# Performance work log

Hardware: AMD Instinct MI355X
Metric: run time of the kernel (lower is better)

Reference implementation:

```python
import jax, jax.numpy as jnp
import numpy as np

# dims
B, N, C_A, C_S, C_Z = 2, 8192, 128, 384, 16
H, D = 4, 32            # n_heads, head_dim (H*D == C_A)
NQ, NK = 32, 128        # local window: queries / keys
NB = 3                  # n_blocks
W = N // NQ             # number of query windows
HID = 2 * C_A           # transition expansion (n=2)


def _ln(x, eps=1e-5):
    # LayerNorm without affine params
    m = jnp.mean(x, axis=-1, keepdims=True)
    v = jnp.var(x, axis=-1, keepdims=True)
    return (x - m) * jax.lax.rsqrt(v + eps)


def setup_inputs() -> dict:
    key = jax.random.key(0)
    ks = iter(jax.random.split(key, 40))
    def rn(shape, scale=1.0):
        return jax.random.normal(next(ks), shape, dtype=jnp.float32) * jnp.float32(scale)
    inp = {
        'q': rn((B, N, C_A)),
        's': rn((B, N, C_S)),
        'p': rn((B, W, NQ, NK, C_Z)),
        # AttentionPairBias (AF3 Alg 24) params, stacked over blocks
        'adaln_scale_w': rn((NB, C_S, C_A), C_S ** -0.5),
        'adaln_scale_b': jnp.zeros((NB, C_A), jnp.float32),
        'adaln_shift_w': rn((NB, C_S, C_A), C_S ** -0.5),
        'wq': rn((NB, C_A, H * D), C_A ** -0.5),
        'bq': jnp.zeros((NB, H * D), jnp.float32),
        'wk': rn((NB, C_A, H * D), C_A ** -0.5),
        'wv': rn((NB, C_A, H * D), C_A ** -0.5),
        'lnz_w': jnp.ones((NB, C_Z), jnp.float32),
        'lnz_b': jnp.zeros((NB, C_Z), jnp.float32),
        'wb_pair': rn((NB, C_Z, H), C_Z ** -0.5),
        'wg': rn((NB, C_A, H * D), C_A ** -0.5),
        'wo': rn((NB, H * D, C_A), (H * D) ** -0.5),
        'sgate_w': rn((NB, C_S, C_A), C_S ** -0.5),
        'sgate_b': jnp.full((NB, C_A), -2.0, jnp.float32),
        # ConditionedTransitionBlock (AF3 Alg 25) params
        't_scale_w': rn((NB, C_S, C_A), C_S ** -0.5),
        't_scale_b': jnp.zeros((NB, C_A), jnp.float32),
        't_shift_w': rn((NB, C_S, C_A), C_S ** -0.5),
        't_wa': rn((NB, C_A, HID), C_A ** -0.5),
        't_wb': rn((NB, C_A, HID), C_A ** -0.5),
        't_wo': rn((NB, HID, C_A), HID ** -0.5),
        't_sgate_w': rn((NB, C_S, C_A), C_S ** -0.5),
        't_sgate_b': jnp.full((NB, C_A), -2.0, jnp.float32),
    }
    return inp


def reference(q, s, p,
              adaln_scale_w, adaln_scale_b, adaln_shift_w,
              wq, bq, wk, wv, lnz_w, lnz_b, wb_pair, wg, wo, sgate_w, sgate_b,
              t_scale_w, t_scale_b, t_shift_w, t_wa, t_wb, t_wo, t_sgate_w, t_sgate_b):
    a = q
    s_ln = _ln(s)  # [B, N, C_S], shared across blocks
    # local window key indices: window w covers queries [w*NQ, (w+1)*NQ), keys
    # are a centered NK-wide window -> offsets in [-(NK-NQ)//2, ...)
    off = (NK - NQ) // 2
    idx = jnp.arange(W)[:, None] * NQ - off + jnp.arange(NK)[None, :]  # [W, NK]
    valid = (idx >= 0) & (idx < N)
    idx_c = jnp.clip(idx, 0, N - 1)
    inv_sqrt_d = jnp.float32(1.0 / np.sqrt(D))
    NEG = jnp.float32(-1e9)

    for i in range(NB):
        # ---- AttentionPairBias (AdaLN-conditioned, pair-biased, gated) ----
        a_ln = _ln(a)
        a_ln = jax.nn.sigmoid(s_ln @ adaln_scale_w[i] + adaln_scale_b[i]) * a_ln \
               + s_ln @ adaln_shift_w[i]
        qh = (a_ln @ wq[i] + bq[i]).reshape(B, N, H, D)
        kh = (a_ln @ wk[i]).reshape(B, N, H, D)
        vh = (a_ln @ wv[i]).reshape(B, N, H, D)
        g = jax.nn.sigmoid(a_ln @ wg[i]).reshape(B, N, H, D)
        # pair bias from z: LN + linear to heads -> [B, W, NQ, NK, H]
        bias = (_ln(p) * lnz_w[i] + lnz_b[i]) @ wb_pair[i]
        qw = qh.reshape(B, W, NQ, H, D)
        kw = kh[:, idx_c]  # [B, W, NK, H, D]
        vw = vh[:, idx_c]
        logits = jnp.einsum('bwqhd,bwkhd->bwqkh', qw, kw) * inv_sqrt_d + bias
        logits = jnp.where(valid[None, :, None, :, None], logits, NEG)
        attn = jax.nn.softmax(logits, axis=3)
        ow = jnp.einsum('bwqkh,bwkhd->bwqhd', attn, vw)
        o = (g * ow.reshape(B, N, H, D)).reshape(B, N, H * D)
        attn_out = (o @ wo[i]) * jax.nn.sigmoid(s_ln @ sgate_w[i] + sgate_b[i])
        # ---- ConditionedTransitionBlock (SwiGLU, sigmoid-gated) ----
        t_ln = _ln(a)
        t_ln = jax.nn.sigmoid(s_ln @ t_scale_w[i] + t_scale_b[i]) * t_ln \
               + s_ln @ t_shift_w[i]
        hidden = jax.nn.silu(t_ln @ t_wa[i]) * (t_ln @ t_wb[i])
        trans_out = (hidden @ t_wo[i]) * jax.nn.sigmoid(s_ln @ t_sgate_w[i] + t_sgate_b[i])
        # AF3 Alg 23: a <- b + ConditionedTransitionBlock(a, s)
        a = attn_out + trans_out
    return a
```

## Files before the change

kernel.cpp:

```cpp
#include <hip/hip_runtime.h>
#include <hip/hip_bf16.h>
#include <cstddef>
#include <cstdint>

#define BB   2
#define NN   8192
#define CA   128
#define CS   384
#define CZ   16
#define HH   4
#define DD   32
#define NQW  32
#define NKW  128
#define NBLK 3
#define WW   256
#define MR   (BB*NN)
#define HIDN 256

typedef unsigned short u16;
typedef __attribute__((ext_vector_type(8))) short short8;
typedef __attribute__((ext_vector_type(4))) float floatx4;

__device__ __forceinline__ float sigmoidf_(float x) { return 1.f / (1.f + __expf(-x)); }

__device__ __forceinline__ u16 f2bf(float x) {
  unsigned u = __float_as_uint(x);
  unsigned r = (u + 0x7fffu + ((u >> 16) & 1u)) >> 16;
  return (u16)r;
}
__device__ __forceinline__ float bf2f(u16 u) {
  return __uint_as_float(((unsigned)u) << 16);
}

__global__ __launch_bounds__(256) void ln_s_kernel(const float* __restrict__ s,
                                                   u16* __restrict__ s_ln_bf) {
  int row  = blockIdx.x * 4 + (threadIdx.x >> 6);
  int lane = threadIdx.x & 63;
  const float* sr = s + (size_t)row * CS;
  float x[6];
  float sum = 0.f, sq = 0.f;
#pragma unroll
  for (int t = 0; t < 6; ++t) { x[t] = sr[lane + 64*t]; sum += x[t]; sq += x[t]*x[t]; }
#pragma unroll
  for (int off = 32; off; off >>= 1) { sum += __shfl_down(sum, off); sq += __shfl_down(sq, off); }
  sum = __shfl(sum, 0); sq = __shfl(sq, 0);
  float mean = sum * (1.f/CS);
  float var  = sq  * (1.f/CS) - mean*mean;
  float rstd = rsqrtf(var + 1e-5f);
  u16* orow = s_ln_bf + (size_t)row * CS;
#pragma unroll
  for (int t = 0; t < 6; ++t) orow[lane + 64*t] = f2bf((x[t]-mean)*rstd);
}

__global__ __launch_bounds__(256) void modln_kernel(const float* __restrict__ a,
                                                    const u16* __restrict__ sp0,
                                                    const u16* __restrict__ sp1,
                                                    const u16* __restrict__ sp3,
                                                    const u16* __restrict__ sp4,
                                                    u16* __restrict__ amod,
                                                    u16* __restrict__ tmod) {
  int row  = blockIdx.x * 4 + (threadIdx.x >> 6);
  int lane = threadIdx.x & 63;
  const float* ar = a + (size_t)row * CA;
  float x0 = ar[lane], x1 = ar[lane + 64];
  float sum = x0 + x1, sq = x0*x0 + x1*x1;
#pragma unroll
  for (int off = 32; off; off >>= 1) { sum += __shfl_down(sum, off); sq += __shfl_down(sq, off); }
  sum = __shfl(sum, 0); sq = __shfl(sq, 0);
  float mean = sum * (1.f/CA);
  float var  = sq  * (1.f/CA) - mean*mean;
  float rstd = rsqrtf(var + 1e-5f);
  float n0 = (x0-mean)*rstd, n1 = (x1-mean)*rstd;
  size_t i0 = (size_t)row * CA + lane;
  amod[i0]      = f2bf(bf2f(sp0[i0])     *n0 + bf2f(sp1[i0]));
  amod[i0 + 64] = f2bf(bf2f(sp0[i0 + 64])*n1 + bf2f(sp1[i0 + 64]));
  tmod[i0]      = f2bf(bf2f(sp3[i0])     *n0 + bf2f(sp4[i0]));
  tmod[i0 + 64] = f2bf(bf2f(sp3[i0 + 64])*n1 + bf2f(sp4[i0 + 64]));
}

struct TJob { const float* src; u16* dst; int K; int N; };
struct TJobs { TJob j[42]; };

__global__ __launch_bounds__(256) void transpose_bf16(TJobs jobs) {
  TJob jb = jobs.j[blockIdx.z];
  int tk = blockIdx.x * 32, tn = blockIdx.y * 32;
  if (tk >= jb.K || tn >= jb.N) return;
  __shared__ float tile[32][33];
  int tx = threadIdx.x & 31;
  int ty = threadIdx.x >> 5;
#pragma unroll
  for (int r = ty; r < 32; r += 8) tile[r][tx] = jb.src[(size_t)(tk + r) * jb.N + tn + tx];
  __syncthreads();
#pragma unroll
  for (int r = ty; r < 32; r += 8)
    jb.dst[(size_t)(tn + r) * jb.K + tk + tx] = f2bf(tile[tx][r]);
}

struct GemmJob {
  const u16* A;
  const u16* Bt;
  const u16* Bt2;
  const float* bias;
  u16* outbf;
  int K;
  int ostride;
  int mode;
  int pad;
};
struct GemmJobs { GemmJob j[18]; };

#define CH_STRIDE 1032

template <bool DUAL>
__global__ __launch_bounds__(256) void gemm_mfma(GemmJobs jobs) {
  GemmJob jb = jobs.j[blockIdx.z];
  const int bm = blockIdx.y * 128, bn = blockIdx.x * 128;
  const int K = jb.K;

  __shared__ u16 As[4 * CH_STRIDE];
  __shared__ u16 Bs[4 * CH_STRIDE];
  __shared__ u16 Bs2[DUAL ? 4 * CH_STRIDE : 8];

  const int tid  = threadIdx.x;
  const int lane = tid & 63;
  const int wave = tid >> 6;
  const int wr = wave >> 1, wc = wave & 1;
  const int l15 = lane & 15, quad = lane >> 4;

  floatx4 acc[4][4] = {};
  floatx4 acc2[DUAL ? 4 : 1][DUAL ? 4 : 1] = {};

  for (int k0 = 0; k0 < K; k0 += 32) {
    __syncthreads();
#pragma unroll
    for (int h = 0; h < 2; ++h) {
      int f = tid + 256 * h;
      int m = f >> 2, c = f & 3;
      uint4 av = *(const uint4*)(jb.A + (size_t)(bm + m) * K + k0 + c * 8);
      *(uint4*)(As + c * CH_STRIDE + m * 8) = av;
      uint4 bv = *(const uint4*)(jb.Bt + (size_t)(bn + m) * K + k0 + c * 8);
      *(uint4*)(Bs + c * CH_STRIDE + m * 8) = bv;
      if constexpr (DUAL) {
        uint4 bv2 = *(const uint4*)(jb.Bt2 + (size_t)(bn + m) * K + k0 + c * 8);
        *(uint4*)(Bs2 + c * CH_STRIDE + m * 8) = bv2;
      }
    }
    __syncthreads();

    short8 a_frag[4], b_frag[4];
#pragma unroll
    for (int mt = 0; mt < 4; ++mt)
      a_frag[mt] = *(const short8*)(As + quad * CH_STRIDE + (wr * 64 + mt * 16 + l15) * 8);
#pragma unroll
    for (int nt = 0; nt < 4; ++nt)
      b_frag[nt] = *(const short8*)(Bs + quad * CH_STRIDE + (wc * 64 + nt * 16 + l15) * 8);
#pragma unroll
    for (int mt = 0; mt < 4; ++mt)
#pragma unroll
      for (int nt = 0; nt < 4; ++nt)
        acc[mt][nt] = __builtin_amdgcn_mfma_f32_16x16x32_bf16(a_frag[mt], b_frag[nt], acc[mt][nt], 0, 0, 0);
    if constexpr (DUAL) {
      short8 b2_frag[4];
#pragma unroll
      for (int nt = 0; nt < 4; ++nt)
        b2_frag[nt] = *(const short8*)(Bs2 + quad * CH_STRIDE + (wc * 64 + nt * 16 + l15) * 8);
#pragma unroll
      for (int mt = 0; mt < 4; ++mt)
#pragma unroll
        for (int nt = 0; nt < 4; ++nt)
          acc2[mt][nt] = __builtin_amdgcn_mfma_f32_16x16x32_bf16(a_frag[mt], b2_frag[nt], acc2[mt][nt], 0, 0, 0);
    }
  }

#pragma unroll
  for (int mt = 0; mt < 4; ++mt) {
#pragma unroll
    for (int nt = 0; nt < 4; ++nt) {
      int n = bn + wc * 64 + nt * 16 + l15;
      int mbase = bm + wr * 64 + mt * 16 + quad * 4;
      floatx4 v = acc[mt][nt];
      if constexpr (DUAL) {
        floatx4 v2 = acc2[mt][nt];
#pragma unroll
        for (int r = 0; r < 4; ++r) {
          size_t idx = (size_t)(mbase + r) * jb.ostride + n;
          float x1 = v[r];
          jb.outbf[idx] = f2bf(x1 * sigmoidf_(x1) * v2[r]);
        }
      } else if (jb.mode == 5) {
        int bidx = mbase >> 13;
        int tok  = mbase & (NN - 1);
        ushort4 o;
        o.x = f2bf(v[0]); o.y = f2bf(v[1]); o.z = f2bf(v[2]); o.w = f2bf(v[3]);
        *(ushort4*)(jb.outbf + (size_t)(bidx * CA + n) * NN + tok) = o;
      } else {
        float bias = jb.bias ? jb.bias[n] : 0.f;
#pragma unroll
        for (int r = 0; r < 4; ++r) {
          size_t idx = (size_t)(mbase + r) * jb.ostride + n;
          float x = v[r] + bias;
          jb.outbf[idx] = f2bf(jb.mode == 1 ? sigmoidf_(x) : x);
        }
      }
    }
  }
}

__global__ __launch_bounds__(256) void combo_kernel(const u16* __restrict__ O,
                                                    const u16* __restrict__ HID,
                                                    const u16* __restrict__ woT,
                                                    const u16* __restrict__ twoT,
                                                    const u16* __restrict__ g1,
                                                    const u16* __restrict__ g2,
                                                    float* __restrict__ outp) {
  const int bm = blockIdx.y * 128;
  __shared__ u16 As[4 * CH_STRIDE];
  __shared__ u16 Bs[4 * CH_STRIDE];
  const int tid  = threadIdx.x;
  const int lane = tid & 63;
  const int wave = tid >> 6;
  const int wr = wave >> 1, wc = wave & 1;
  const int l15 = lane & 15, quad = lane >> 4;

  floatx4 acc1[4][4] = {};
  floatx4 acc2[4][4] = {};

  for (int k0 = 0; k0 < CA; k0 += 32) {
    __syncthreads();
#pragma unroll
    for (int h = 0; h < 2; ++h) {
      int f = tid + 256 * h;
      int m = f >> 2, c = f & 3;
      *(uint4*)(As + c * CH_STRIDE + m * 8) = *(const uint4*)(O + (size_t)(bm + m) * CA + k0 + c * 8);
      *(uint4*)(Bs + c * CH_STRIDE + m * 8) = *(const uint4*)(woT + (size_t)m * CA + k0 + c * 8);
    }
    __syncthreads();
    short8 a_frag[4], b_frag[4];
#pragma unroll
    for (int mt = 0; mt < 4; ++mt)
      a_frag[mt] = *(const short8*)(As + quad * CH_STRIDE + (wr * 64 + mt * 16 + l15) * 8);
#pragma unroll
    for (int nt = 0; nt < 4; ++nt)
      b_frag[nt] = *(const short8*)(Bs + quad * CH_STRIDE + (wc * 64 + nt * 16 + l15) * 8);
#pragma unroll
    for (int mt = 0; mt < 4; ++mt)
#pragma unroll
      for (int nt = 0; nt < 4; ++nt)
        acc1[mt][nt] = __builtin_amdgcn_mfma_f32_16x16x32_bf16(a_frag[mt], b_frag[nt], acc1[mt][nt], 0, 0, 0);
  }
  for (int k0 = 0; k0 < HIDN; k0 += 32) {
    __syncthreads();
#pragma unroll
    for (int h = 0; h < 2; ++h) {
      int f = tid + 256 * h;
      int m = f >> 2, c = f & 3;
      *(uint4*)(As + c * CH_STRIDE + m * 8) = *(const uint4*)(HID + (size_t)(bm + m) * HIDN + k0 + c * 8);
      *(uint4*)(Bs + c * CH_STRIDE + m * 8) = *(const uint4*)(twoT + (size_t)m * HIDN + k0 + c * 8);
    }
    __syncthreads();
    short8 a_frag[4], b_frag[4];
#pragma unroll
    for (int mt = 0; mt < 4; ++mt)
      a_frag[mt] = *(const short8*)(As + quad * CH_STRIDE + (wr * 64 + mt * 16 + l15) * 8);
#pragma unroll
    for (int nt = 0; nt < 4; ++nt)
      b_frag[nt] = *(const short8*)(Bs + quad * CH_STRIDE + (wc * 64 + nt * 16 + l15) * 8);
#pragma unroll
    for (int mt = 0; mt < 4; ++mt)
#pragma unroll
      for (int nt = 0; nt < 4; ++nt)
        acc2[mt][nt] = __builtin_amdgcn_mfma_f32_16x16x32_bf16(a_frag[mt], b_frag[nt], acc2[mt][nt], 0, 0, 0);
  }

#pragma unroll
  for (int mt = 0; mt < 4; ++mt) {
#pragma unroll
    for (int nt = 0; nt < 4; ++nt) {
      int n = wc * 64 + nt * 16 + l15;
      int mbase = bm + wr * 64 + mt * 16 + quad * 4;
#pragma unroll
      for (int r = 0; r < 4; ++r) {
        size_t idx = (size_t)(mbase + r) * CA + n;
        outp[idx] = acc1[mt][nt][r] * bf2f(g1[idx]) + acc2[mt][nt][r] * bf2f(g2[idx]);
      }
    }
  }
}

__global__ __launch_bounds__(256) void bias3_kernel(const float* __restrict__ p,
                                                    const float* __restrict__ lnz_w,
                                                    const float* __restrict__ lnz_b,
                                                    const float* __restrict__ wb,
                                                    u16* __restrict__ biasT) {
  const int kc = blockIdx.x, w = blockIdx.y, b = blockIdx.z;
  __shared__ float effW[12][16];
  __shared__ float effb[12];
  const int t = threadIdx.x;
  if (t < 192) {
    int i = t >> 6, rem = t & 63, z = rem >> 2, hh = rem & 3;
    effW[i*4 + hh][z] = lnz_w[i*CZ + z] * wb[(i*CZ + z)*HH + hh];
  }
  if (t < 12) {
    int i = t >> 2, hh = t & 3;
    float acc = 0.f;
    for (int z = 0; z < 16; ++z) acc += lnz_b[i*CZ + z] * wb[(i*CZ + z)*HH + hh];
    effb[t] = acc;
  }
  __syncthreads();

  const int kk = t & 31, qg = (t >> 5) * 4;
  const int k = kc * 32 + kk;
  u16 out4[12][4];
#pragma unroll
  for (int r = 0; r < 4; ++r) {
    int qq = qg + r;
    const float4* pr = (const float4*)(p + (size_t)(((b * WW + w) * NQW + qq) * NKW + k) * 16);
    float4 p0 = pr[0], p1 = pr[1], p2 = pr[2], p3 = pr[3];
    float x[16] = {p0.x,p0.y,p0.z,p0.w, p1.x,p1.y,p1.z,p1.w,
                   p2.x,p2.y,p2.z,p2.w, p3.x,p3.y,p3.z,p3.w};
    float sum = 0.f, sq = 0.f;
#pragma unroll
    for (int z = 0; z < 16; ++z) { sum += x[z]; sq += x[z]*x[z]; }
    float mean = sum * (1.f/16.f);
    float var  = sq  * (1.f/16.f) - mean*mean;
    float rstd = rsqrtf(var + 1e-5f);
#pragma unroll
    for (int ih = 0; ih < 12; ++ih) {
      float acc = effb[ih];
#pragma unroll
      for (int z = 0; z < 16; ++z) acc += (x[z]-mean)*rstd * effW[ih][z];
      out4[ih][r] = f2bf(acc);
    }
  }
#pragma unroll
  for (int ih = 0; ih < 12; ++ih) {
    int i = ih >> 2, hh = ih & 3;
    u16* dst = biasT + ((((size_t)i * BB + b) * WW + w) * HH + hh) * 4096 + (size_t)k * 32 + qg;
    ushort4 uv; uv.x = out4[ih][0]; uv.y = out4[ih][1]; uv.z = out4[ih][2]; uv.w = out4[ih][3];
    *(ushort4*)dst = uv;
  }
}

__global__ __launch_bounds__(64) void attn_mfma(const u16* __restrict__ Qb,
                                                const u16* __restrict__ Kb,
                                                const u16* __restrict__ Vtb,
                                                const u16* __restrict__ Gb,
                                                const u16* __restrict__ biasT,
                                                u16* __restrict__ Ob) {
  const int w = blockIdx.x, h = blockIdx.y, b = blockIdx.z;
  __shared__ u16 Pt[128 * 36];
  __shared__ float inv_s[32];
  const int lane = threadIdx.x;
  const int l15 = lane & 15, quad = lane >> 4;
  const int tok0 = w * NQW - 48;

  short8 qf[2];
#pragma unroll
  for (int mt = 0; mt < 2; ++mt) {
    int qq = w * NQW + mt * 16 + l15;
    qf[mt] = *(const short8*)(Qb + (size_t)(b * NN + qq) * CA + h * DD + quad * 8);
  }
  floatx4 lg[2][8] = {};
#pragma unroll
  for (int nt = 0; nt < 8; ++nt) {
    int tk = tok0 + nt * 16 + l15;
    int tc = min(max(tk, 0), NN - 1);
    short8 kf = *(const short8*)(Kb + (size_t)(b * NN + tc) * CA + h * DD + quad * 8);
#pragma unroll
    for (int mt = 0; mt < 2; ++mt)
      lg[mt][nt] = __builtin_amdgcn_mfma_f32_16x16x32_bf16(qf[mt], kf, lg[mt][nt], 0, 0, 0);
  }

  const float scale = 0.17677669529663687f;
  const u16* bb = biasT + ((((size_t)b * WW + w) * HH + h) << 12);
  float mrow[2][4];
#pragma unroll
  for (int mt = 0; mt < 2; ++mt)
#pragma unroll
    for (int r = 0; r < 4; ++r) mrow[mt][r] = -3.0e38f;
#pragma unroll
  for (int nt = 0; nt < 8; ++nt) {
    int tk = tok0 + nt * 16 + l15;
    bool valid = (tk >= 0) && (tk < NN);
#pragma unroll
    for (int mt = 0; mt < 2; ++mt) {
      ushort4 bv = *(const ushort4*)(bb + (nt * 16 + l15) * 32 + mt * 16 + quad * 4);
      float bvf[4] = {bf2f(bv.x), bf2f(bv.y), bf2f(bv.z), bf2f(bv.w)};
#pragma unroll
      for (int r = 0; r < 4; ++r) {
        float l = valid ? (lg[mt][nt][r] * scale + bvf[r]) : -1e9f;
        lg[mt][nt][r] = l;
        mrow[mt][r] = fmaxf(mrow[mt][r], l);
      }
    }
  }
#pragma unroll
  for (int mt = 0; mt < 2; ++mt)
#pragma unroll
    for (int r = 0; r < 4; ++r) {
      float m = mrow[mt][r];
      m = fmaxf(m, __shfl_xor(m, 1));
      m = fmaxf(m, __shfl_xor(m, 2));
      m = fmaxf(m, __shfl_xor(m, 4));
      m = fmaxf(m, __shfl_xor(m, 8));
      mrow[mt][r] = m;
    }

  float srow[2][4] = {};
#pragma unroll
  for (int nt = 0; nt < 8; ++nt)
#pragma unroll
    for (int mt = 0; mt < 2; ++mt) {
      u16 pv[4];
#pragma unroll
      for (int r = 0; r < 4; ++r) {
        float e = __expf(lg[mt][nt][r] - mrow[mt][r]);
        srow[mt][r] += e;
        pv[r] = f2bf(e);
      }
      ushort4 uv; uv.x = pv[0]; uv.y = pv[1]; uv.z = pv[2]; uv.w = pv[3];
      *(ushort4*)(Pt + (nt * 16 + l15) * 36 + mt * 16 + quad * 4) = uv;
    }
#pragma unroll
  for (int mt = 0; mt < 2; ++mt)
#pragma unroll
    for (int r = 0; r < 4; ++r) {
      float ssum = srow[mt][r];
      ssum += __shfl_xor(ssum, 1);
      ssum += __shfl_xor(ssum, 2);
      ssum += __shfl_xor(ssum, 4);
      ssum += __shfl_xor(ssum, 8);
      if (l15 == 0) inv_s[mt * 16 + quad * 4 + r] = 1.f / ssum;
    }
  __syncthreads();

  floatx4 oacc[2][2] = {};
#pragma unroll
  for (int ks = 0; ks < 4; ++ks) {
    short8 pf[2];
#pragma unroll
    for (int ntq = 0; ntq < 2; ++ntq)
#pragma unroll
      for (int j = 0; j < 8; ++j)
        pf[ntq][j] = (short)Pt[(ks * 32 + quad * 8 + j) * 36 + ntq * 16 + l15];
    int tb = tok0 + ks * 32 + quad * 8;
    tb = min(max(tb, 0), NN - 8);
#pragma unroll
    for (int mtd = 0; mtd < 2; ++mtd) {
      short8 vf = *(const short8*)(Vtb + (size_t)(b * CA + h * DD + mtd * 16 + l15) * NN + tb);
#pragma unroll
      for (int ntq = 0; ntq < 2; ++ntq)
        oacc[mtd][ntq] = __builtin_amdgcn_mfma_f32_16x16x32_bf16(vf, pf[ntq], oacc[mtd][ntq], 0, 0, 0);
    }
  }

#pragma unroll
  for (int mtd = 0; mtd < 2; ++mtd)
#pragma unroll
    for (int ntq = 0; ntq < 2; ++ntq) {
      int qq = ntq * 16 + l15;
      float inv = inv_s[qq];
      int tok = w * NQW + qq;
      size_t base = (size_t)(b * NN + tok) * CA + h * DD + mtd * 16 + quad * 4;
      ushort4 gv = *(const ushort4*)(Gb + base);
      floatx4 v = oacc[mtd][ntq];
      ushort4 o;
      o.x = f2bf(bf2f(gv.x) * v[0] * inv);
      o.y = f2bf(bf2f(gv.y) * v[1] * inv);
      o.z = f2bf(bf2f(gv.z) * v[2] * inv);
      o.w = f2bf(bf2f(gv.w) * v[3] * inv);
      *(ushort4*)(Ob + base) = o;
    }
}

extern "C" void kernel_launch(void* const* d_in, const int* in_sizes, int n_in,
                              void* d_out, int out_size, void* d_ws, size_t ws_size,
                              hipStream_t stream) {
  const float* q             = (const float*)d_in[0];
  const float* s             = (const float*)d_in[1];
  const float* p             = (const float*)d_in[2];
  const float* adaln_scale_w = (const float*)d_in[3];
  const float* adaln_scale_b = (const float*)d_in[4];
  const float* adaln_shift_w = (const float*)d_in[5];
  const float* wq            = (const float*)d_in[6];
  const float* bq            = (const float*)d_in[7];
  const float* wk            = (const float*)d_in[8];
  const float* wv            = (const float*)d_in[9];
  const float* lnz_w         = (const float*)d_in[10];
  const float* lnz_b         = (const float*)d_in[11];
  const float* wb_pair       = (const float*)d_in[12];
  const float* wg            = (const float*)d_in[13];
  const float* wo            = (const float*)d_in[14];
  const float* sgate_w       = (const float*)d_in[15];
  const float* sgate_b       = (const float*)d_in[16];
  const float* t_scale_w     = (const float*)d_in[17];
  const float* t_scale_b     = (const float*)d_in[18];
  const float* t_shift_w     = (const float*)d_in[19];
  const float* t_wa          = (const float*)d_in[20];
  const float* t_wb          = (const float*)d_in[21];
  const float* t_wo          = (const float*)d_in[22];
  const float* t_sgate_w     = (const float*)d_in[23];
  const float* t_sgate_b     = (const float*)d_in[24];
  float* out = (float*)d_out;

  const size_t MC = (size_t)MR * CA;
  float* fws   = (float*)d_ws;
  float* abuf0 = fws;
  float* abuf1 = abuf0 + MC;
  u16* uws     = (u16*)(abuf1 + MC);
  u16* s_ln_bf = uws;
  u16* SP      = s_ln_bf + (size_t)MR * CS;
  u16* amod    = SP + 18*MC;
  u16* tmod    = amod + MC;
  u16* Qb      = tmod + MC;
  u16* Kb      = Qb + MC;
  u16* Vtb     = Kb + MC;
  u16* Gb      = Vtb + MC;
  u16* Ob      = Gb + MC;
  u16* HIDb    = Ob + MC;
  u16* biasT   = HIDb + 2*MC;
  u16* wbuf    = biasT + (size_t)3*BB*WW*HH*NQW*NKW;

  const size_t WBLK = 6*(size_t)CA*CS + 5*(size_t)CA*CA + 3*(size_t)CA*HIDN;
  const size_t o_ascale = 0;
  const size_t o_ashift = o_ascale + (size_t)CA*CS;
  const size_t o_sgate  = o_ashift + (size_t)CA*CS;
  const size_t o_tscale = o_sgate  + (size_t)CA*CS;
  const size_t o_tshift = o_tscale + (size_t)CA*CS;
  const size_t o_tsgate = o_tshift + (size_t)CA*CS;
  const size_t o_wq     = o_tsgate + (size_t)CA*CS;
  const size_t o_wk     = o_wq + (size_t)CA*CA;
  const size_t o_wv     = o_wk + (size_t)CA*CA;
  const size_t o_wg     = o_wv + (size_t)CA*CA;
  const size_t o_wo     = o_wg + (size_t)CA*CA;
  const size_t o_twa    = o_wo + (size_t)CA*CA;
  const size_t o_twb    = o_twa + (size_t)HIDN*CA;
  const size_t o_two    = o_twb + (size_t)HIDN*CA;

  ln_s_kernel<<<MR/4, 256, 0, stream>>>(s, s_ln_bf);

  TJobs tj;
  for (int i = 0; i < NBLK; ++i) {
    u16* wb0 = wbuf + (size_t)i * WBLK;
    int b14 = i * 14;
    tj.j[b14+0]  = TJob{adaln_scale_w + (size_t)i*CS*CA, wb0 + o_ascale, CS, CA};
    tj.j[b14+1]  = TJob{adaln_shift_w + (size_t)i*CS*CA, wb0 + o_ashift, CS, CA};
    tj.j[b14+2]  = TJob{sgate_w       + (size_t)i*CS*CA, wb0 + o_sgate,  CS, CA};
    tj.j[b14+3]  = TJob{t_scale_w     + (size_t)i*CS*CA, wb0 + o_tscale, CS, CA};
    tj.j[b14+4]  = TJob{t_shift_w     + (size_t)i*CS*CA, wb0 + o_tshift, CS, CA};
    tj.j[b14+5]  = TJob{t_sgate_w     + (size_t)i*CS*CA, wb0 + o_tsgate, CS, CA};
    tj.j[b14+6]  = TJob{wq   + (size_t)i*CA*CA,   wb0 + o_wq,  CA, CA};
    tj.j[b14+7]  = TJob{wk   + (size_t)i*CA*CA,   wb0 + o_wk,  CA, CA};
    tj.j[b14+8]  = TJob{wv   + (size_t)i*CA*CA,   wb0 + o_wv,  CA, CA};
    tj.j[b14+9]  = TJob{wg   + (size_t)i*CA*CA,   wb0 + o_wg,  CA, CA};
    tj.j[b14+10] = TJob{wo   + (size_t)i*CA*CA,   wb0 + o_wo,  CA, CA};
    tj.j[b14+11] = TJob{t_wa + (size_t)i*CA*HIDN, wb0 + o_twa, CA, HIDN};
    tj.j[b14+12] = TJob{t_wb + (size_t)i*CA*HIDN, wb0 + o_twb, CA, HIDN};
    tj.j[b14+13] = TJob{t_wo + (size_t)i*HIDN*CA, wb0 + o_two, HIDN, CA};
  }
  transpose_bf16<<<dim3(12, 8, 42), 256, 0, stream>>>(tj);

  bias3_kernel<<<dim3(4, WW, BB), 256, 0, stream>>>(p, lnz_w, lnz_b, wb_pair, biasT);

  {
    GemmJobs js = {};
    for (int i = 0; i < NBLK; ++i) {
      u16* wb0 = wbuf + (size_t)i * WBLK;
      js.j[i*6+0] = GemmJob{s_ln_bf, wb0 + o_ascale, nullptr, adaln_scale_b + i*CA, SP + (i*6+0)*MC, CS, CA, 1, 0};
      js.j[i*6+1] = GemmJob{s_ln_bf, wb0 + o_ashift, nullptr, nullptr,              SP + (i*6+1)*MC, CS, CA, 0, 0};
      js.j[i*6+2] = GemmJob{s_ln_bf, wb0 + o_sgate,  nullptr, sgate_b   + i*CA,     SP + (i*6+2)*MC, CS, CA, 1, 0};
      js.j[i*6+3] = GemmJob{s_ln_bf, wb0 + o_tscale, nullptr, t_scale_b + i*CA,     SP + (i*6+3)*MC, CS, CA, 1, 0};
      js.j[i*6+4] = GemmJob{s_ln_bf, wb0 + o_tshift, nullptr, nullptr,              SP + (i*6+4)*MC, CS, CA, 0, 0};
      js.j[i*6+5] = GemmJob{s_ln_bf, wb0 + o_tsgate, nullptr, t_sgate_b + i*CA,     SP + (i*6+5)*MC, CS, CA, 1, 0};
    }
    gemm_mfma<false><<<dim3(1, MR/128, 18), 256, 0, stream>>>(js);
  }

  for (int i = 0; i < NBLK; ++i) {
    const float* a_in = (i == 0) ? q : (i == 1 ? abuf0 : abuf1);
    float* a_out = (i == 2) ? out : (i == 0 ? abuf0 : abuf1);
    u16* wb0 = wbuf + (size_t)i * WBLK;

    modln_kernel<<<MR/4, 256, 0, stream>>>(a_in, SP + (i*6+0)*MC, SP + (i*6+1)*MC,
                                           SP + (i*6+3)*MC, SP + (i*6+4)*MC, amod, tmod);

    GemmJobs jq = {};
    jq.j[0] = GemmJob{amod, wb0 + o_wq, nullptr, bq + i*CA, Qb,  CA, CA, 0, 0};
    jq.j[1] = GemmJob{amod, wb0 + o_wk, nullptr, nullptr,   Kb,  CA, CA, 0, 0};
    jq.j[2] = GemmJob{amod, wb0 + o_wv, nullptr, nullptr,   Vtb, CA, CA, 5, 0};
    jq.j[3] = GemmJob{amod, wb0 + o_wg, nullptr, nullptr,   Gb,  CA, CA, 1, 0};
    gemm_mfma<false><<<dim3(1, MR/128, 4), 256, 0, stream>>>(jq);

    GemmJobs jh = {};
    jh.j[0] = GemmJob{tmod, wb0 + o_twa, wb0 + o_twb, nullptr, HIDb, CA, HIDN, 4, 0};
    gemm_mfma<true><<<dim3(2, MR/128, 1), 256, 0, stream>>>(jh);

    attn_mfma<<<dim3(WW, HH, BB), 64, 0, stream>>>(
        Qb, Kb, Vtb, Gb, biasT + (size_t)i * BB*WW*HH*4096, Ob);

    combo_kernel<<<dim3(1, MR/128), 256, 0, stream>>>(
        Ob, HIDb, wb0 + o_wo, wb0 + o_two,
        SP + (i*6+2)*MC, SP + (i*6+5)*MC, a_out);
  }
}
```

Before: 548.1 us.

## Fuse next-block modulated LayerNorm into combo epilogue and use direct global-to-LDS loads

```diff
diff --git a/kernel.cpp b/kernel.cpp
--- a/kernel.cpp
+++ b/kernel.cpp
@@ -32,6 +32,12 @@
   return __uint_as_float(((unsigned)u) << 16);
 }
 
+typedef const unsigned int __attribute__((address_space(1)))* gas_t;
+typedef unsigned int __attribute__((address_space(3)))* las_t;
+__device__ __forceinline__ void gload16(const u16* gp, u16* lds_wave_base) {
+  __builtin_amdgcn_global_load_lds((gas_t)(const void*)gp, (las_t)(void*)lds_wave_base, 16, 0, 0);
+}
+
 __global__ __launch_bounds__(256) void ln_s_kernel(const float* __restrict__ s,
                                                    u16* __restrict__ s_ln_bf) {
   int row  = blockIdx.x * 4 + (threadIdx.x >> 6);
@@ -109,17 +115,15 @@
 };
 struct GemmJobs { GemmJob j[18]; };
 
-#define CH_STRIDE 1032
-
 template <bool DUAL>
 __global__ __launch_bounds__(256) void gemm_mfma(GemmJobs jobs) {
   GemmJob jb = jobs.j[blockIdx.z];
   const int bm = blockIdx.y * 128, bn = blockIdx.x * 128;
   const int K = jb.K;
 
-  __shared__ u16 As[4 * CH_STRIDE];
-  __shared__ u16 Bs[4 * CH_STRIDE];
-  __shared__ u16 Bs2[DUAL ? 4 * CH_STRIDE : 8];
+  __shared__ __attribute__((aligned(16))) u16 As[4096];
+  __shared__ __attribute__((aligned(16))) u16 Bs[4096];
+  __shared__ __attribute__((aligned(16))) u16 Bs2[DUAL ? 4096 : 8];
 
   const int tid  = threadIdx.x;
   const int lane = tid & 63;
@@ -135,25 +139,22 @@
 #pragma unroll
     for (int h = 0; h < 2; ++h) {
       int f = tid + 256 * h;
-      int m = f >> 2, c = f & 3;
-      uint4 av = *(const uint4*)(jb.A + (size_t)(bm + m) * K + k0 + c * 8);
-      *(uint4*)(As + c * CH_STRIDE + m * 8) = av;
-      uint4 bv = *(const uint4*)(jb.Bt + (size_t)(bn + m) * K + k0 + c * 8);
-      *(uint4*)(Bs + c * CH_STRIDE + m * 8) = bv;
-      if constexpr (DUAL) {
-        uint4 bv2 = *(const uint4*)(jb.Bt2 + (size_t)(bn + m) * K + k0 + c * 8);
-        *(uint4*)(Bs2 + c * CH_STRIDE + m * 8) = bv2;
-      }
+      int m = f >> 2, c = (f & 3) * 8;
+      int lbase = (wave * 64 + 256 * h) * 8;
+      gload16(jb.A  + (size_t)(bm + m) * K + k0 + c, As + lbase);
+      gload16(jb.Bt + (size_t)(bn + m) * K + k0 + c, Bs + lbase);
+      if constexpr (DUAL)
+        gload16(jb.Bt2 + (size_t)(bn + m) * K + k0 + c, Bs2 + lbase);
     }
     __syncthreads();
 
     short8 a_frag[4], b_frag[4];
 #pragma unroll
     for (int mt = 0; mt < 4; ++mt)
-      a_frag[mt] = *(const short8*)(As + quad * CH_STRIDE + (wr * 64 + mt * 16 + l15) * 8);
+      a_frag[mt] = *(const short8*)(As + (wr * 64 + mt * 16 + l15) * 32 + quad * 8);
 #pragma unroll
     for (int nt = 0; nt < 4; ++nt)
-      b_frag[nt] = *(const short8*)(Bs + quad * CH_STRIDE + (wc * 64 + nt * 16 + l15) * 8);
+      b_frag[nt] = *(const short8*)(Bs + (wc * 64 + nt * 16 + l15) * 32 + quad * 8);
 #pragma unroll
     for (int mt = 0; mt < 4; ++mt)
 #pragma unroll
@@ -163,7 +164,7 @@
       short8 b2_frag[4];
 #pragma unroll
       for (int nt = 0; nt < 4; ++nt)
-        b2_frag[nt] = *(const short8*)(Bs2 + quad * CH_STRIDE + (wc * 64 + nt * 16 + l15) * 8);
+        b2_frag[nt] = *(const short8*)(Bs2 + (wc * 64 + nt * 16 + l15) * 32 + quad * 8);
 #pragma unroll
       for (int mt = 0; mt < 4; ++mt)
 #pragma unroll
@@ -206,16 +207,26 @@
   }
 }
 
+template <bool FINAL>
 __global__ __launch_bounds__(256) void combo_kernel(const u16* __restrict__ O,
                                                     const u16* __restrict__ HID,
                                                     const u16* __restrict__ woT,
                                                     const u16* __restrict__ twoT,
                                                     const u16* __restrict__ g1,
                                                     const u16* __restrict__ g2,
+                                                    const u16* __restrict__ sp0,
+                                                    const u16* __restrict__ sp1,
+                                                    const u16* __restrict__ sp3,
+                                                    const u16* __restrict__ sp4,
+                                                    u16* __restrict__ amod,
+                                                    u16* __restrict__ tmod,
                                                     float* __restrict__ outp) {
   const int bm = blockIdx.y * 128;
-  __shared__ u16 As[4 * CH_STRIDE];
-  __shared__ u16 Bs[4 * CH_STRIDE];
+  __shared__ __attribute__((aligned(16))) u16 As[4096];
+  __shared__ __attribute__((aligned(16))) u16 Bs[4096];
+  __shared__ float redS[2][128];
+  __shared__ float redQ[2][128];
+  __shared__ float stats[128][2];
   const int tid  = threadIdx.x;
   const int lane = tid & 63;
   const int wave = tid >> 6;
@@ -230,18 +241,19 @@
 #pragma unroll
     for (int h = 0; h < 2; ++h) {
       int f = tid + 256 * h;
-      int m = f >> 2, c = f & 3;
-      *(uint4*)(As + c * CH_STRIDE + m * 8) = *(const uint4*)(O + (size_t)(bm + m) * CA + k0 + c * 8);
-      *(uint4*)(Bs + c * CH_STRIDE + m * 8) = *(const uint4*)(woT + (size_t)m * CA + k0 + c * 8);
+      int m = f >> 2, c = (f & 3) * 8;
+      int lbase = (wave * 64 + 256 * h) * 8;
+      gload16(O   + (size_t)(bm + m) * CA + k0 + c, As + lbase);
+      gload16(woT + (size_t)m * CA + k0 + c, Bs + lbase);
     }
     __syncthreads();
     short8 a_frag[4], b_frag[4];
 #pragma unroll
     for (int mt = 0; mt < 4; ++mt)
-      a_frag[mt] = *(const short8*)(As + quad * CH_STRIDE + (wr * 64 + mt * 16 + l15) * 8);
+      a_frag[mt] = *(const short8*)(As + (wr * 64 + mt * 16 + l15) * 32 + quad * 8);
 #pragma unroll
     for (int nt = 0; nt < 4; ++nt)
-      b_frag[nt] = *(const short8*)(Bs + quad * CH_STRIDE + (wc * 64 + nt * 16 + l15) * 8);
+      b_frag[nt] = *(const short8*)(Bs + (wc * 64 + nt * 16 + l15) * 32 + quad * 8);
 #pragma unroll
     for (int mt = 0; mt < 4; ++mt)
 #pragma unroll
@@ -253,18 +265,19 @@
 #pragma unroll
     for (int h = 0; h < 2; ++h) {
       int f = tid + 256 * h;
-      int m = f >> 2, c = f & 3;
-      *(uint4*)(As + c * CH_STRIDE + m * 8) = *(const uint4*)(HID + (size_t)(bm + m) * HIDN + k0 + c * 8);
-      *(uint4*)(Bs + c * CH_STRIDE + m * 8) = *(const uint4*)(twoT + (size_t)m * HIDN + k0 + c * 8);
+      int m = f >> 2, c = (f & 3) * 8;
+      int lbase = (wave * 64 + 256 * h) * 8;
+      gload16(HID  + (size_t)(bm + m) * HIDN + k0 + c, As + lbase);
+      gload16(twoT + (size_t)m * HIDN + k0 + c, Bs + lbase);
     }
     __syncthreads();
     short8 a_frag[4], b_frag[4];
 #pragma unroll
     for (int mt = 0; mt < 4; ++mt)
-      a_frag[mt] = *(const short8*)(As + quad * CH_STRIDE + (wr * 64 + mt * 16 + l15) * 8);
+      a_frag[mt] = *(const short8*)(As + (wr * 64 + mt * 16 + l15) * 32 + quad * 8);
 #pragma unroll
     for (int nt = 0; nt < 4; ++nt)
-      b_frag[nt] = *(const short8*)(Bs + quad * CH_STRIDE + (wc * 64 + nt * 16 + l15) * 8);
+      b_frag[nt] = *(const short8*)(Bs + (wc * 64 + nt * 16 + l15) * 32 + quad * 8);
 #pragma unroll
     for (int mt = 0; mt < 4; ++mt)
 #pragma unroll
@@ -281,9 +294,71 @@
 #pragma unroll
       for (int r = 0; r < 4; ++r) {
         size_t idx = (size_t)(mbase + r) * CA + n;
-        outp[idx] = acc1[mt][nt][r] * bf2f(g1[idx]) + acc2[mt][nt][r] * bf2f(g2[idx]);
+        acc1[mt][nt][r] = acc1[mt][nt][r] * bf2f(g1[idx]) + acc2[mt][nt][r] * bf2f(g2[idx]);
       }
     }
+  }
+
+  if constexpr (FINAL) {
+#pragma unroll
+    for (int mt = 0; mt < 4; ++mt)
+#pragma unroll
+      for (int nt = 0; nt < 4; ++nt) {
+        int n = wc * 64 + nt * 16 + l15;
+        int mbase = bm + wr * 64 + mt * 16 + quad * 4;
+#pragma unroll
+        for (int r = 0; r < 4; ++r)
+          outp[(size_t)(mbase + r) * CA + n] = acc1[mt][nt][r];
+      }
+  } else {
+    float ps[4][4], pq[4][4];
+#pragma unroll
+    for (int mt = 0; mt < 4; ++mt)
+#pragma unroll
+      for (int r = 0; r < 4; ++r) {
+        float s = 0.f, q2 = 0.f;
+#pragma unroll
+        for (int nt = 0; nt < 4; ++nt) { float v = acc1[mt][nt][r]; s += v; q2 += v*v; }
+#pragma unroll
+        for (int d = 1; d < 16; d <<= 1) { s += __shfl_xor(s, d); q2 += __shfl_xor(q2, d); }
+        ps[mt][r] = s; pq[mt][r] = q2;
+      }
+    __syncthreads();
+    if (l15 == 0) {
+#pragma unroll
+      for (int mt = 0; mt < 4; ++mt)
+#pragma unroll
+        for (int r = 0; r < 4; ++r) {
+          int row = wr * 64 + mt * 16 + quad * 4 + r;
+          redS[wc][row] = ps[mt][r];
+          redQ[wc][row] = pq[mt][r];
+        }
+    }
+    __syncthreads();
+    if (tid < 128) {
+      float s  = redS[0][tid] + redS[1][tid];
+      float q2 = redQ[0][tid] + redQ[1][tid];
+      float mean = s * (1.f/CA);
+      float var  = q2 * (1.f/CA) - mean*mean;
+      stats[tid][0] = mean;
+      stats[tid][1] = rsqrtf(var + 1e-5f);
+    }
+    __syncthreads();
+#pragma unroll
+    for (int mt = 0; mt < 4; ++mt)
+#pragma unroll
+      for (int nt = 0; nt < 4; ++nt) {
+        int n = wc * 64 + nt * 16 + l15;
+        int rowb = wr * 64 + mt * 16 + quad * 4;
+#pragma unroll
+        for (int r = 0; r < 4; ++r) {
+          float mean = stats[rowb + r][0], rstd = stats[rowb + r][1];
+          float nx = (acc1[mt][nt][r] - mean) * rstd;
+          size_t idx = (size_t)(bm + rowb + r) * CA + n;
+          amod[idx] = f2bf(bf2f(sp0[idx]) * nx + bf2f(sp1[idx]));
+          tmod[idx] = f2bf(bf2f(sp3[idx]) * nx + bf2f(sp4[idx]));
+        }
+      }
   }
 }
 
@@ -504,10 +579,7 @@
   float* out = (float*)d_out;
 
   const size_t MC = (size_t)MR * CA;
-  float* fws   = (float*)d_ws;
-  float* abuf0 = fws;
-  float* abuf1 = abuf0 + MC;
-  u16* uws     = (u16*)(abuf1 + MC);
+  u16* uws     = (u16*)d_ws;
   u16* s_ln_bf = uws;
   u16* SP      = s_ln_bf + (size_t)MR * CS;
   u16* amod    = SP + 18*MC;
@@ -576,13 +648,11 @@
     gemm_mfma<false><<<dim3(1, MR/128, 18), 256, 0, stream>>>(js);
   }
 
+  modln_kernel<<<MR/4, 256, 0, stream>>>(q, SP + 0*MC, SP + 1*MC, SP + 3*MC, SP + 4*MC,
+                                         amod, tmod);
+
   for (int i = 0; i < NBLK; ++i) {
-    const float* a_in = (i == 0) ? q : (i == 1 ? abuf0 : abuf1);
-    float* a_out = (i == 2) ? out : (i == 0 ? abuf0 : abuf1);
     u16* wb0 = wbuf + (size_t)i * WBLK;
-
-    modln_kernel<<<MR/4, 256, 0, stream>>>(a_in, SP + (i*6+0)*MC, SP + (i*6+1)*MC,
-                                           SP + (i*6+3)*MC, SP + (i*6+4)*MC, amod, tmod);
 
     GemmJobs jq = {};
     jq.j[0] = GemmJob{amod, wb0 + o_wq, nullptr, bq + i*CA, Qb,  CA, CA, 0, 0};
@@ -598,8 +668,19 @@
     attn_mfma<<<dim3(WW, HH, BB), 64, 0, stream>>>(
         Qb, Kb, Vtb, Gb, biasT + (size_t)i * BB*WW*HH*4096, Ob);
 
-    combo_kernel<<<dim3(1, MR/128), 256, 0, stream>>>(
-        Ob, HIDb, wb0 + o_wo, wb0 + o_two,
-        SP + (i*6+2)*MC, SP + (i*6+5)*MC, a_out);
-  }
-}
+    if (i < 2) {
+      combo_kernel<false><<<dim3(1, MR/128), 256, 0, stream>>>(
+          Ob, HIDb, wb0 + o_wo, wb0 + o_two,
+          SP + (i*6+2)*MC, SP + (i*6+5)*MC,
+          SP + ((i+1)*6+0)*MC, SP + ((i+1)*6+1)*MC,
+          SP + ((i+1)*6+3)*MC, SP + ((i+1)*6+4)*MC,
+          amod, tmod, nullptr);
+    } else {
+      combo_kernel<true><<<dim3(1, MR/128), 256, 0, stream>>>(
+          Ob, HIDb, wb0 + o_wo, wb0 + o_two,
+          SP + (i*6+2)*MC, SP + (i*6+5)*MC,
+          nullptr, nullptr, nullptr, nullptr,
+          nullptr, nullptr, out);
+    }
+  }
+}
```

New measurement: 548.2 us. Within noise of the previous version (+0.0%).
